# Performance work log

Measured on AMD Instinct MI355X. Metric: run time of the kernel, lower is better.

Reference implementation:

```python
import jax, jax.numpy as jnp
import numpy as np

B, T, D_MODEL, D_STATE = 8, 2048, 1024, 256


def setup_inputs() -> dict:
    key = jax.random.key(0)
    ks = jax.random.split(key, 11)
    def lecun(k, shape):
        fan_in = shape[0]
        return jax.random.normal(k, shape, jnp.float32) / jnp.sqrt(jnp.float32(fan_in))
    return {
        "x": jax.random.normal(ks[0], (B, T, D_MODEL), jnp.float32),
        "W_in": lecun(ks[1], (D_MODEL, D_STATE)),
        "b_in": jnp.zeros((D_STATE,), jnp.float32),
        "W_gate": lecun(ks[2], (D_MODEL, D_MODEL)),
        "b_gate": jnp.zeros((D_MODEL,), jnp.float32),
        "A": lecun(ks[3], (D_STATE, D_STATE)),
        "Bm": lecun(ks[4], (D_STATE, D_STATE)),
        "C": lecun(ks[5], (D_MODEL, D_STATE)),
        "D": lecun(ks[6], (D_MODEL, D_STATE)),
        "W_out": lecun(ks[7], (D_MODEL, D_MODEL)),
        "b_out": jnp.zeros((D_MODEL,), jnp.float32),
    }


def reference(x, W_in, b_in, W_gate, b_gate, A, Bm, C, D, W_out, b_out):
    b, t, d_model = x.shape
    d_state = A.shape[0]
    u = x @ W_in + b_in                      # [B,T,d_state]
    g = jax.nn.sigmoid(x @ W_gate + b_gate)  # [B,T,d_model]

    u_seq = jnp.swapaxes(u, 0, 1)  # [T,B,d_state]
    g_seq = jnp.swapaxes(g, 0, 1)  # [T,B,d_model]
    x_seq = jnp.swapaxes(x, 0, 1)  # [T,B,d_model]

    def step(h_prev, inputs):
        u_t, g_t, x_t = inputs
        h_t = jnp.tanh(h_prev @ A + u_t @ Bm)            # [B,d_state]
        y_t = h_t @ C.T + u_t @ D.T                      # [B,d_model]
        y_t = g_t * y_t + (1.0 - g_t) * x_t
        return h_t, y_t

    h0 = jnp.zeros((b, d_state), x.dtype)
    _, ys = jax.lax.scan(step, h0, xs=(u_seq, g_seq, x_seq))
    ys = jnp.swapaxes(ys, 0, 1)  # [B,T,d_model]
    return ys @ W_out + b_out + x
```

## Files before the change

kernel.cpp:

```cpp
#include <hip/hip_runtime.h>
#include <math.h>


enum { E_NONE = 0, E_BIASBF = 1, E_SIGBF = 2, E_ACC = 3, E_BIASRES = 4, E_CVTBF = 5 };

typedef __attribute__((ext_vector_type(8))) short bf16x8;
typedef __attribute__((ext_vector_type(4))) float f32x4;

static __device__ inline unsigned short f2bf(float f) {
    unsigned u = __builtin_bit_cast(unsigned, f);
    unsigned r = (u + 0x7fff + ((u >> 16) & 1)) >> 16;
    return (unsigned short)r;
}
static __device__ inline unsigned pack2(float a, float b) {
    return (unsigned)f2bf(a) | ((unsigned)f2bf(b) << 16);
}
static __device__ inline float bflo(unsigned u) {
    return __builtin_bit_cast(float, u << 16);
}
static __device__ inline float bfhi(unsigned u) {
    return __builtin_bit_cast(float, u & 0xffff0000u);
}
static __device__ inline float tanh_fast(float x) {
    float e = __builtin_amdgcn_exp2f(x * 2.8853900817779268f);
    float t = __builtin_amdgcn_rcpf(e + 1.0f);
    return fmaf(-2.0f, t, 1.0f);
}

__global__ __launch_bounds__(256) void cvt_bf(
    const float* __restrict__ in, unsigned short* __restrict__ out, int n8)
{
    int i = blockIdx.x * 256 + threadIdx.x;
    if (i >= n8) return;
    float4 a = ((const float4*)in)[i * 2];
    float4 b = ((const float4*)in)[i * 2 + 1];
    uint4 o;
    o.x = pack2(a.x, a.y); o.y = pack2(a.z, a.w);
    o.z = pack2(b.x, b.y); o.w = pack2(b.z, b.w);
    ((uint4*)out)[i] = o;
}

__global__ __launch_bounds__(256) void transpose_bf(
    const float* __restrict__ in, unsigned short* __restrict__ out, int R, int C)
{
    __shared__ float tile[32][33];
    const int bx = blockIdx.x * 32, by = blockIdx.y * 32;
    const int tx = threadIdx.x & 31, ty = threadIdx.x >> 5;
#pragma unroll
    for (int i = 0; i < 32; i += 8)
        tile[ty + i][tx] = in[(size_t)(by + ty + i) * C + bx + tx];
    __syncthreads();
#pragma unroll
    for (int i = 0; i < 32; i += 8)
        out[(size_t)(bx + ty + i) * R + by + tx] = f2bf(tile[tx][ty + i]);
}

template <int EPI>
__global__ __launch_bounds__(256) void gemm_mfma(
    const unsigned short* __restrict__ Ag,
    const unsigned short* __restrict__ Bg,
    const float* __restrict__ bias, const float* __restrict__ res,
    void* Cg, int M, int N, int K)
{
    __shared__ __align__(16) unsigned char Lds[2][32768];
    const int tid = threadIdx.x;
    const int w = tid >> 6, l = tid & 63;
    const int r = l & 15, g = l >> 4;
    const int m0 = blockIdx.y * 128, n0 = blockIdx.x * 128;

    const unsigned char* agp[4];
    const unsigned char* bgp[4];
#pragma unroll
    for (int j = 0; j < 4; ++j) {
        const int c = w * 256 + j * 64 + l;
        const int row = c >> 3;
        const unsigned offp = ((unsigned)(c & 7) * 16u) ^ ((unsigned)(row & 7) * 16u);
        agp[j] = (const unsigned char*)Ag + ((size_t)(m0 + row) * K) * 2 + offp;
        bgp[j] = (const unsigned char*)Bg + ((size_t)(n0 + row) * K) * 2 + offp;
    }

#define STAGE(BUF)                                                            \
    {                                                                         \
      _Pragma("unroll")                                                       \
      for (int j = 0; j < 4; ++j) {                                           \
        __builtin_amdgcn_global_load_lds(                                     \
            (const __attribute__((address_space(1))) unsigned*)(agp[j]),      \
            (__attribute__((address_space(3))) unsigned*)&Lds[(BUF)][w * 4096 + j * 1024], \
            16, 0, 0);                                                        \
        __builtin_amdgcn_global_load_lds(                                     \
            (const __attribute__((address_space(1))) unsigned*)(bgp[j]),      \
            (__attribute__((address_space(3))) unsigned*)&Lds[(BUF)][16384 + w * 4096 + j * 1024], \
            16, 0, 0);                                                        \
        agp[j] += 128; bgp[j] += 128;                                         \
      }                                                                       \
    }

    f32x4 acc[2][8];
#pragma unroll
    for (int mt = 0; mt < 2; ++mt)
#pragma unroll
        for (int nt = 0; nt < 8; ++nt) acc[mt][nt] = (f32x4){0.f, 0.f, 0.f, 0.f};

    const int nk = K >> 6;
    STAGE(0)
    __syncthreads();
    for (int t = 0; t < nk; ++t) {
        const int buf = t & 1;
        if (t + 1 < nk) { STAGE(buf ^ 1) }
        bf16x8 af[2][2], bfr[8][2];
#pragma unroll
        for (int s = 0; s < 2; ++s) {
#pragma unroll
            for (int mt = 0; mt < 2; ++mt) {
                const int row = w * 32 + mt * 16 + r;
                af[mt][s] = *(const bf16x8*)&Lds[buf][row * 128 +
                    ((s * 64 + 16 * g) ^ (16 * (row & 7)))];
            }
#pragma unroll
            for (int nt = 0; nt < 8; ++nt) {
                const int row = nt * 16 + r;
                bfr[nt][s] = *(const bf16x8*)&Lds[buf][16384 + row * 128 +
                    ((s * 64 + 16 * g) ^ (16 * (row & 7)))];
            }
        }
#pragma unroll
        for (int s = 0; s < 2; ++s)
#pragma unroll
            for (int mt = 0; mt < 2; ++mt)
#pragma unroll
                for (int nt = 0; nt < 8; ++nt)
                    acc[mt][nt] = __builtin_amdgcn_mfma_f32_16x16x32_bf16(
                        af[mt][s], bfr[nt][s], acc[mt][nt], 0, 0, 0);
        __syncthreads();
    }
#undef STAGE

#pragma unroll
    for (int mt = 0; mt < 2; ++mt)
#pragma unroll
        for (int nt = 0; nt < 8; ++nt) {
            const int n = n0 + nt * 16 + r;
            float bv = 0.f;
            if (EPI == E_BIASBF || EPI == E_SIGBF || EPI == E_BIASRES) bv = bias[n];
#pragma unroll
            for (int q = 0; q < 4; ++q) {
                const int m = m0 + w * 32 + mt * 16 + g * 4 + q;
                const size_t idx = (size_t)m * N + n;
                float v = acc[mt][nt][q] + bv;
                if (EPI == E_SIGBF) v = 1.f / (1.f + expf(-v));
                if (EPI == E_ACC) v += ((const float*)Cg)[idx];
                if (EPI == E_BIASRES) v += res[idx];
                if (EPI == E_BIASBF || EPI == E_SIGBF || EPI == E_CVTBF)
                    ((unsigned short*)Cg)[idx] = f2bf(v);
                else
                    ((float*)Cg)[idx] = v;
            }
        }
}

__global__ __launch_bounds__(256, 1) void scan_mfma(
    const float* __restrict__ Amat, const unsigned short* __restrict__ u2bf,
    unsigned short* __restrict__ hbf)
{
    constexpr int T = 2048;
    constexpr int NCH = T / 8;
    __shared__ __align__(16) unsigned char LDSM[8192 + 2 * 4096];
    unsigned char* Hb = LDSM;
    unsigned char* Ub = LDSM + 8192;

    const int tid = threadIdx.x;
    const int bb = blockIdx.x;
    const int w = tid >> 6, l = tid & 63;
    const int r = l & 15, g = l >> 4;
    const int m0 = w * 64;
    const bool c1 = (r & 1) != 0, c2 = (r & 2) != 0;

    if (tid < 128) ((unsigned*)Hb)[tid] = 0u;

    bf16x8 af[4][8];
#pragma unroll
    for (int mt = 0; mt < 4; ++mt) {
        const int m = m0 + mt * 16 + r;
#pragma unroll
        for (int kt = 0; kt < 8; ++kt) {
            unsigned wd[4];
#pragma unroll
            for (int jw = 0; jw < 4; ++jw) {
                const int k = kt * 32 + g * 8 + jw * 2;
                wd[jw] = pack2(Amat[(size_t)k * 256 + m],
                               Amat[(size_t)(k + 1) * 256 + m]);
            }
            af[mt][kt] = __builtin_bit_cast(bf16x8, *(uint4*)wd);
        }
    }

    const unsigned char* u2b = (const unsigned char*)u2bf + (size_t)bb * T * 512;
    unsigned short* hb = hbf + (size_t)bb * T * 256;

    __builtin_amdgcn_global_load_lds(
        (const __attribute__((address_space(1))) unsigned*)(u2b + tid * 16),
        (__attribute__((address_space(3))) unsigned*)(Ub + tid * 16), 16, 0, 0);
    __builtin_amdgcn_global_load_lds(
        (const __attribute__((address_space(1))) unsigned*)(u2b + 4096 + tid * 16),
        (__attribute__((address_space(3))) unsigned*)(Ub + 4096 + tid * 16), 16, 0, 0);
    asm volatile("s_waitcnt vmcnt(0) lgkmcnt(0)" ::: "memory");
    __builtin_amdgcn_sched_barrier(0);
    __builtin_amdgcn_s_barrier();
    __builtin_amdgcn_sched_barrier(0);

#define SCAN_STEP(I)                                                          \
  {                                                                           \
    bf16x8 hf[8];                                                             \
    _Pragma("unroll")                                                         \
    for (int kt = 0; kt < 8; ++kt)                                            \
      hf[kt] = *(const bf16x8*)(Hb + c15 + (I) * 512u +                       \
                                (unsigned)(kt * 64 + g * 16));                \
    float uu[4];                                                              \
    _Pragma("unroll")                                                         \
    for (int mt = 0; mt < 4; ++mt) {                                          \
      unsigned short us = *(const unsigned short*)(                           \
          Uc + (I) * 512u + (unsigned)((m0 + mt * 16 + g * 4 + (r & 3)) * 2));\
      uu[mt] = bflo(us);                                                      \
    }                                                                         \
    asm volatile("s_waitcnt lgkmcnt(0)" ::: "memory");                        \
    __builtin_amdgcn_sched_barrier(0);                                        \
    f32x4 p0[4], p1[4];                                                       \
    _Pragma("unroll")                                                         \
    for (int mt = 0; mt < 4; ++mt) {                                          \
      p0[mt] = (f32x4){0.f, 0.f, 0.f, 0.f};                                   \
      p1[mt] = (f32x4){0.f, 0.f, 0.f, 0.f};                                   \
    }                                                                         \
    _Pragma("unroll")                                                         \
    for (int kt = 0; kt < 4; ++kt) {                                          \
      _Pragma("unroll")                                                       \
      for (int mt = 0; mt < 4; ++mt) {                                        \
        p0[mt] = __builtin_amdgcn_mfma_f32_16x16x32_bf16(af[mt][kt], hf[kt],  \
                                                         p0[mt], 0, 0, 0);    \
        p1[mt] = __builtin_amdgcn_mfma_f32_16x16x32_bf16(                     \
            af[mt][kt + 4], hf[kt + 4], p1[mt], 0, 0, 0);                     \
      }                                                                       \
    }                                                                         \
    const unsigned bwb = ((I) == 7) ? (c15 ^ 4096u) : (c15 + ((I) + 1) * 512u);\
    _Pragma("unroll")                                                         \
    for (int mt = 0; mt < 4; ++mt) {                                          \
      float s0 = p0[mt][0] + p1[mt][0];                                       \
      float s1 = p0[mt][1] + p1[mt][1];                                       \
      float s2 = p0[mt][2] + p1[mt][2];                                       \
      float s3 = p0[mt][3] + p1[mt][3];                                       \
      float sv = c2 ? (c1 ? s3 : s2) : (c1 ? s1 : s0);                        \
      float hv = tanh_fast(sv + uu[mt]);                                      \
      unsigned pk;                                                            \
      asm("v_cvt_pk_bf16_f32 %0, %1, %2" : "=v"(pk) : "v"(hv), "v"(hv));      \
      if (r < 4)                                                              \
        *(unsigned short*)(Hb + bwb +                                         \
            (unsigned)((m0 + mt * 16 + g * 4 + r) * 2)) = (unsigned short)pk; \
    }                                                                         \
    asm volatile("s_waitcnt lgkmcnt(0)" ::: "memory");                        \
    __builtin_amdgcn_sched_barrier(0);                                        \
    __builtin_amdgcn_s_barrier();                                             \
    __builtin_amdgcn_sched_barrier(0);                                        \
  }

    for (int chunk = 0; chunk < NCH; ++chunk) {
        const int t0 = chunk * 8;
        const unsigned c15 = (unsigned)(t0 & 15) * 512u;
        unsigned char* Uc = Ub + ((unsigned)(chunk & 1) << 12);

        SCAN_STEP(0)
        SCAN_STEP(1)
        SCAN_STEP(2)
        SCAN_STEP(3)
        SCAN_STEP(4)
        SCAN_STEP(5)
        SCAN_STEP(6)
        SCAN_STEP(7)

        {
            const int flat = tid * 16;
            const int i = flat >> 9, byte = flat & 511;
            const int slot = (t0 + 1 + i) & 15;
            uint4 dat = *(const uint4*)(Hb + slot * 512 + byte);
            *(uint4*)((unsigned char*)hb + (size_t)(t0 + i) * 512 + byte) = dat;
        }
        if (chunk + 2 < NCH) {
            __builtin_amdgcn_global_load_lds(
                (const __attribute__((address_space(1))) unsigned*)(
                    u2b + (size_t)(t0 + 16) * 512 + tid * 16),
                (__attribute__((address_space(3))) unsigned*)(
                    Ub + ((unsigned)(chunk & 1) << 12) + tid * 16), 16, 0, 0);
            asm volatile("s_waitcnt vmcnt(2)" ::: "memory");
        } else {
            asm volatile("s_waitcnt vmcnt(1)" ::: "memory");
        }
        __builtin_amdgcn_sched_barrier(0);
        __builtin_amdgcn_s_barrier();
        __builtin_amdgcn_sched_barrier(0);
    }
#undef SCAN_STEP
}

__global__ __launch_bounds__(256) void ewise(
    const unsigned short* __restrict__ g8, const float* __restrict__ big,
    const float* __restrict__ x, unsigned short* __restrict__ ys, int n8)
{
    int i = blockIdx.x * 256 + threadIdx.x;
    if (i >= n8) return;
    uint4 gv = ((const uint4*)g8)[i];
    float4 b0 = ((const float4*)big)[i * 2], b1 = ((const float4*)big)[i * 2 + 1];
    float4 x0 = ((const float4*)x)[i * 2], x1 = ((const float4*)x)[i * 2 + 1];
    float gg[8] = {bflo(gv.x), bfhi(gv.x), bflo(gv.y), bfhi(gv.y),
                   bflo(gv.z), bfhi(gv.z), bflo(gv.w), bfhi(gv.w)};
    float bb[8] = {b0.x, b0.y, b0.z, b0.w, b1.x, b1.y, b1.z, b1.w};
    float xx[8] = {x0.x, x0.y, x0.z, x0.w, x1.x, x1.y, x1.z, x1.w};
    float yy[8];
#pragma unroll
    for (int k = 0; k < 8; ++k) yy[k] = gg[k] * bb[k] + (1.f - gg[k]) * xx[k];
    uint4 o;
    o.x = pack2(yy[0], yy[1]); o.y = pack2(yy[2], yy[3]);
    o.z = pack2(yy[4], yy[5]); o.w = pack2(yy[6], yy[7]);
    ((uint4*)ys)[i] = o;
}

extern "C" void kernel_launch(void* const* d_in, const int* in_sizes, int n_in,
                              void* d_out, int out_size, void* d_ws, size_t ws_size,
                              hipStream_t stream)
{
    const float* x      = (const float*)d_in[0];
    const float* W_in   = (const float*)d_in[1];
    const float* b_in   = (const float*)d_in[2];
    const float* W_gate = (const float*)d_in[3];
    const float* b_gate = (const float*)d_in[4];
    const float* Amat   = (const float*)d_in[5];
    const float* Bm     = (const float*)d_in[6];
    const float* Cm     = (const float*)d_in[7];
    const float* Dm     = (const float*)d_in[8];
    const float* W_out  = (const float*)d_in[9];
    const float* b_out  = (const float*)d_in[10];

    const int T = 2048, DM = 1024, DS = 256;
    const int M = 8 * T;
    const size_t MB = 1024 * 1024;
    char* ws = (char*)d_ws;

    unsigned short* xbf  = (unsigned short*)(ws);
    unsigned short* ysbf = xbf;
    unsigned short* u    = (unsigned short*)(ws + 32 * MB);
    unsigned short* u2   = (unsigned short*)(ws + 40 * MB);
    unsigned short* h    = (unsigned short*)(ws + 56 * MB);
    unsigned short* WinT = (unsigned short*)(ws + 64 * MB);
    unsigned short* BmT  = (unsigned short*)(ws + 64 * MB + 512 * 1024);
    unsigned short* WgT  = (unsigned short*)(ws + 65 * MB);
    unsigned short* WoT  = (unsigned short*)(ws + 67 * MB);
    unsigned short* Cbf  = (unsigned short*)(ws + 69 * MB);
    unsigned short* Dbf  = (unsigned short*)(ws + 69 * MB + 512 * 1024);
    float*          big  = (float*)(ws + 70 * MB);
    unsigned short* gbf  = (unsigned short*)(ws + 134 * MB);

    cvt_bf<<<M * DM / 8 / 256, 256, 0, stream>>>(x, xbf, M * DM / 8);
    transpose_bf<<<dim3(DS / 32, DM / 32), 256, 0, stream>>>(W_in, WinT, DM, DS);
    transpose_bf<<<dim3(DS / 32, DS / 32), 256, 0, stream>>>(Bm, BmT, DS, DS);
    transpose_bf<<<dim3(DM / 32, DM / 32), 256, 0, stream>>>(W_gate, WgT, DM, DM);
    transpose_bf<<<dim3(DM / 32, DM / 32), 256, 0, stream>>>(W_out, WoT, DM, DM);
    cvt_bf<<<DM * DS / 8 / 256, 256, 0, stream>>>(Cm, Cbf, DM * DS / 8);
    cvt_bf<<<DM * DS / 8 / 256, 256, 0, stream>>>(Dm, Dbf, DM * DS / 8);

    gemm_mfma<E_BIASBF><<<dim3(DS / 128, M / 128), 256, 0, stream>>>(
        xbf, WinT, b_in, nullptr, u, M, DS, DM);
    gemm_mfma<E_NONE><<<dim3(DM / 128, M / 128), 256, 0, stream>>>(
        u, Dbf, nullptr, nullptr, big, M, DM, DS);
    gemm_mfma<E_CVTBF><<<dim3(DS / 128, M / 128), 256, 0, stream>>>(
        u, BmT, nullptr, nullptr, u2, M, DS, DS);
    gemm_mfma<E_SIGBF><<<dim3(DM / 128, M / 128), 256, 0, stream>>>(
        xbf, WgT, b_gate, nullptr, gbf, M, DM, DM);
    scan_mfma<<<8, 256, 0, stream>>>(Amat, u2, h);
    gemm_mfma<E_ACC><<<dim3(DM / 128, M / 128), 256, 0, stream>>>(
        h, Cbf, nullptr, nullptr, big, M, DM, DS);
    ewise<<<M * DM / 8 / 256, 256, 0, stream>>>(gbf, big, x, ysbf, M * DM / 8);
    gemm_mfma<E_BIASRES><<<dim3(DM / 128, M / 128), 256, 0, stream>>>(
        ysbf, WoT, b_out, x, (float*)d_out, M, DM, DM);
}
```

Before: 1.559 ms.

## Interleave two batch recurrences per scan workgroup to hide MFMA latency

The scan kernel now processes two independent batch sequences per workgroup, launching 4 blocks instead of 8. Each step issues the MFMA chains for both sequences back to back, so one chain's latency can overlap the other, and the two sequences share a single barrier per step. The cost is double the per-step work on each block, more LDS and registers, and half as many compute units in use.

```diff
diff --git a/kernel.cpp b/kernel.cpp
--- a/kernel.cpp
+++ b/kernel.cpp
@@ -164,18 +164,23 @@
 {
     constexpr int T = 2048;
     constexpr int NCH = T / 8;
-    __shared__ __align__(16) unsigned char LDSM[8192 + 2 * 4096];
-    unsigned char* Hb = LDSM;
-    unsigned char* Ub = LDSM + 8192;
+    __shared__ __align__(16) unsigned char LDSM[4 * 8192];
+    unsigned char* HbA = LDSM;
+    unsigned char* HbB = LDSM + 8192;
+    unsigned char* UA  = LDSM + 16384;
+    unsigned char* UB  = LDSM + 24576;
 
     const int tid = threadIdx.x;
-    const int bb = blockIdx.x;
+    const int p = blockIdx.x;
     const int w = tid >> 6, l = tid & 63;
     const int r = l & 15, g = l >> 4;
     const int m0 = w * 64;
     const bool c1 = (r & 1) != 0, c2 = (r & 2) != 0;
 
-    if (tid < 128) ((unsigned*)Hb)[tid] = 0u;
+    if (tid < 128) {
+        ((unsigned*)HbA)[tid] = 0u;
+        ((unsigned*)HbB)[tid] = 0u;
+    }
 
     bf16x8 af[4][8];
 #pragma unroll
@@ -194,66 +199,97 @@
         }
     }
 
-    const unsigned char* u2b = (const unsigned char*)u2bf + (size_t)bb * T * 512;
-    unsigned short* hb = hbf + (size_t)bb * T * 256;
-
-    __builtin_amdgcn_global_load_lds(
-        (const __attribute__((address_space(1))) unsigned*)(u2b + tid * 16),
-        (__attribute__((address_space(3))) unsigned*)(Ub + tid * 16), 16, 0, 0);
-    __builtin_amdgcn_global_load_lds(
-        (const __attribute__((address_space(1))) unsigned*)(u2b + 4096 + tid * 16),
-        (__attribute__((address_space(3))) unsigned*)(Ub + 4096 + tid * 16), 16, 0, 0);
-    asm volatile("s_waitcnt vmcnt(0) lgkmcnt(0)" ::: "memory");
+    const unsigned char* uAsrc = (const unsigned char*)u2bf + (size_t)(2 * p) * T * 512;
+    const unsigned char* uBsrc = (const unsigned char*)u2bf + (size_t)(2 * p + 1) * T * 512;
+    unsigned char* hAdst = (unsigned char*)(hbf + (size_t)(2 * p) * T * 256);
+    unsigned char* hBdst = (unsigned char*)(hbf + (size_t)(2 * p + 1) * T * 256);
+
+#pragma unroll
+    for (int buf = 0; buf < 2; ++buf) {
+        __builtin_amdgcn_global_load_lds(
+            (const __attribute__((address_space(1))) unsigned*)(uAsrc + buf * 4096 + tid * 16),
+            (__attribute__((address_space(3))) unsigned*)(UA + buf * 4096 + tid * 16), 16, 0, 0);
+        __builtin_amdgcn_global_load_lds(
+            (const __attribute__((address_space(1))) unsigned*)(uBsrc + buf * 4096 + tid * 16),
+            (__attribute__((address_space(3))) unsigned*)(UB + buf * 4096 + tid * 16), 16, 0, 0);
+    }
+    asm volatile("s_waitcnt vmcnt(2) lgkmcnt(0)" ::: "memory");
     __builtin_amdgcn_sched_barrier(0);
     __builtin_amdgcn_s_barrier();
     __builtin_amdgcn_sched_barrier(0);
 
+    unsigned uo[4];
+#pragma unroll
+    for (int mt = 0; mt < 4; ++mt)
+        uo[mt] = (unsigned)((m0 + mt * 16 + g * 4 + (r & 3)) * 2);
+
+#define CHAIN(HB, UC, PF0, PF1, US)                                           \
+    {                                                                         \
+      _Pragma("unroll")                                                       \
+      for (int mt = 0; mt < 4; ++mt) {                                        \
+        PF0[mt] = (f32x4){0.f, 0.f, 0.f, 0.f};                                \
+        PF1[mt] = (f32x4){0.f, 0.f, 0.f, 0.f};                                \
+      }                                                                       \
+    }
+
 #define SCAN_STEP(I)                                                          \
   {                                                                           \
-    bf16x8 hf[8];                                                             \
+    const unsigned ro = c15 + (I) * 512u;                                     \
+    const unsigned bwb = ((I) == 7) ? (c15 ^ 4096u) : (c15 + ((I) + 1) * 512u);\
+    bf16x8 hfA[8], hfB[8];                                                    \
     _Pragma("unroll")                                                         \
     for (int kt = 0; kt < 8; ++kt)                                            \
-      hf[kt] = *(const bf16x8*)(Hb + c15 + (I) * 512u +                       \
-                                (unsigned)(kt * 64 + g * 16));                \
-    float uu[4];                                                              \
+      hfA[kt] = *(const bf16x8*)(HbA + ro + (unsigned)(kt * 64 + g * 16));    \
+    _Pragma("unroll")                                                         \
+    for (int kt = 0; kt < 8; ++kt)                                            \
+      hfB[kt] = *(const bf16x8*)(HbB + ro + (unsigned)(kt * 64 + g * 16));    \
+    unsigned short usA[4], usB[4];                                            \
     _Pragma("unroll")                                                         \
     for (int mt = 0; mt < 4; ++mt) {                                          \
-      unsigned short us = *(const unsigned short*)(                           \
-          Uc + (I) * 512u + (unsigned)((m0 + mt * 16 + g * 4 + (r & 3)) * 2));\
-      uu[mt] = bflo(us);                                                      \
+      usA[mt] = *(const unsigned short*)(UcA + (I) * 512u + uo[mt]);          \
+      usB[mt] = *(const unsigned short*)(UcB + (I) * 512u + uo[mt]);          \
     }                                                                         \
-    asm volatile("s_waitcnt lgkmcnt(0)" ::: "memory");                        \
-    __builtin_amdgcn_sched_barrier(0);                                        \
-    f32x4 p0[4], p1[4];                                                       \
-    _Pragma("unroll")                                                         \
-    for (int mt = 0; mt < 4; ++mt) {                                          \
-      p0[mt] = (f32x4){0.f, 0.f, 0.f, 0.f};                                   \
-      p1[mt] = (f32x4){0.f, 0.f, 0.f, 0.f};                                   \
-    }                                                                         \
+    f32x4 pA0[4], pA1[4], pB0[4], pB1[4];                                     \
+    CHAIN(HbA, UcA, pA0, pA1, usA)                                            \
+    CHAIN(HbB, UcB, pB0, pB1, usB)                                            \
     _Pragma("unroll")                                                         \
     for (int kt = 0; kt < 4; ++kt) {                                          \
       _Pragma("unroll")                                                       \
       for (int mt = 0; mt < 4; ++mt) {                                        \
-        p0[mt] = __builtin_amdgcn_mfma_f32_16x16x32_bf16(af[mt][kt], hf[kt],  \
-                                                         p0[mt], 0, 0, 0);    \
-        p1[mt] = __builtin_amdgcn_mfma_f32_16x16x32_bf16(                     \
-            af[mt][kt + 4], hf[kt + 4], p1[mt], 0, 0, 0);                     \
+        pA0[mt] = __builtin_amdgcn_mfma_f32_16x16x32_bf16(af[mt][kt], hfA[kt],\
+                                                          pA0[mt], 0, 0, 0);  \
+        pA1[mt] = __builtin_amdgcn_mfma_f32_16x16x32_bf16(                    \
+            af[mt][kt + 4], hfA[kt + 4], pA1[mt], 0, 0, 0);                   \
       }                                                                       \
     }                                                                         \
-    const unsigned bwb = ((I) == 7) ? (c15 ^ 4096u) : (c15 + ((I) + 1) * 512u);\
+    _Pragma("unroll")                                                         \
+    for (int kt = 0; kt < 4; ++kt) {                                          \
+      _Pragma("unroll")                                                       \
+      for (int mt = 0; mt < 4; ++mt) {                                        \
+        pB0[mt] = __builtin_amdgcn_mfma_f32_16x16x32_bf16(af[mt][kt], hfB[kt],\
+                                                          pB0[mt], 0, 0, 0);  \
+        pB1[mt] = __builtin_amdgcn_mfma_f32_16x16x32_bf16(                    \
+            af[mt][kt + 4], hfB[kt + 4], pB1[mt], 0, 0, 0);                   \
+      }                                                                       \
+    }                                                                         \
     _Pragma("unroll")                                                         \
     for (int mt = 0; mt < 4; ++mt) {                                          \
-      float s0 = p0[mt][0] + p1[mt][0];                                       \
-      float s1 = p0[mt][1] + p1[mt][1];                                       \
-      float s2 = p0[mt][2] + p1[mt][2];                                       \
-      float s3 = p0[mt][3] + p1[mt][3];                                       \
-      float sv = c2 ? (c1 ? s3 : s2) : (c1 ? s1 : s0);                        \
-      float hv = tanh_fast(sv + uu[mt]);                                      \
-      unsigned pk;                                                            \
-      asm("v_cvt_pk_bf16_f32 %0, %1, %2" : "=v"(pk) : "v"(hv), "v"(hv));      \
-      if (r < 4)                                                              \
-        *(unsigned short*)(Hb + bwb +                                         \
-            (unsigned)((m0 + mt * 16 + g * 4 + r) * 2)) = (unsigned short)pk; \
+      float a0 = pA0[mt][0] + pA1[mt][0], a1 = pA0[mt][1] + pA1[mt][1];       \
+      float a2 = pA0[mt][2] + pA1[mt][2], a3 = pA0[mt][3] + pA1[mt][3];       \
+      float sa = c2 ? (c1 ? a3 : a2) : (c1 ? a1 : a0);                        \
+      float ha = tanh_fast(sa + bflo((unsigned)usA[mt]));                     \
+      float b0 = pB0[mt][0] + pB1[mt][0], b1 = pB0[mt][1] + pB1[mt][1];       \
+      float b2 = pB0[mt][2] + pB1[mt][2], b3 = pB0[mt][3] + pB1[mt][3];       \
+      float sb = c2 ? (c1 ? b3 : b2) : (c1 ? b1 : b0);                        \
+      float hbv = tanh_fast(sb + bflo((unsigned)usB[mt]));                    \
+      unsigned pka, pkb;                                                      \
+      asm("v_cvt_pk_bf16_f32 %0, %1, %2" : "=v"(pka) : "v"(ha), "v"(ha));     \
+      asm("v_cvt_pk_bf16_f32 %0, %1, %2" : "=v"(pkb) : "v"(hbv), "v"(hbv));   \
+      if (r < 4) {                                                            \
+        const unsigned wb = bwb + (unsigned)((m0 + mt * 16 + g * 4 + r) * 2); \
+        *(unsigned short*)(HbA + wb) = (unsigned short)pka;                   \
+        *(unsigned short*)(HbB + wb) = (unsigned short)pkb;                   \
+      }                                                                       \
     }                                                                         \
     asm volatile("s_waitcnt lgkmcnt(0)" ::: "memory");                        \
     __builtin_amdgcn_sched_barrier(0);                                        \
@@ -264,7 +300,8 @@
     for (int chunk = 0; chunk < NCH; ++chunk) {
         const int t0 = chunk * 8;
         const unsigned c15 = (unsigned)(t0 & 15) * 512u;
-        unsigned char* Uc = Ub + ((unsigned)(chunk & 1) << 12);
+        const unsigned char* UcA = UA + ((unsigned)(chunk & 1) << 12);
+        const unsigned char* UcB = UB + ((unsigned)(chunk & 1) << 12);
 
         SCAN_STEP(0)
         SCAN_STEP(1)
@@ -276,27 +313,34 @@
         SCAN_STEP(7)
 
         {
-            const int flat = tid * 16;
-            const int i = flat >> 9, byte = flat & 511;
+            const int i = tid >> 5;
+            const int byte = (tid & 31) * 16;
             const int slot = (t0 + 1 + i) & 15;
-            uint4 dat = *(const uint4*)(Hb + slot * 512 + byte);
-            *(uint4*)((unsigned char*)hb + (size_t)(t0 + i) * 512 + byte) = dat;
+            uint4 da = *(const uint4*)(HbA + slot * 512 + byte);
+            uint4 db = *(const uint4*)(HbB + slot * 512 + byte);
+            *(uint4*)(hAdst + (size_t)(t0 + i) * 512 + byte) = da;
+            *(uint4*)(hBdst + (size_t)(t0 + i) * 512 + byte) = db;
         }
         if (chunk + 2 < NCH) {
+            const unsigned nb = (unsigned)(chunk & 1) << 12;
             __builtin_amdgcn_global_load_lds(
                 (const __attribute__((address_space(1))) unsigned*)(
-                    u2b + (size_t)(t0 + 16) * 512 + tid * 16),
-                (__attribute__((address_space(3))) unsigned*)(
-                    Ub + ((unsigned)(chunk & 1) << 12) + tid * 16), 16, 0, 0);
+                    uAsrc + (size_t)(t0 + 16) * 512 + tid * 16),
+                (__attribute__((address_space(3))) unsigned*)(UA + nb + tid * 16), 16, 0, 0);
+            __builtin_amdgcn_global_load_lds(
+                (const __attribute__((address_space(1))) unsigned*)(
+                    uBsrc + (size_t)(t0 + 16) * 512 + tid * 16),
+                (__attribute__((address_space(3))) unsigned*)(UB + nb + tid * 16), 16, 0, 0);
+            asm volatile("s_waitcnt vmcnt(4)" ::: "memory");
+        } else {
             asm volatile("s_waitcnt vmcnt(2)" ::: "memory");
-        } else {
-            asm volatile("s_waitcnt vmcnt(1)" ::: "memory");
         }
         __builtin_amdgcn_sched_barrier(0);
         __builtin_amdgcn_s_barrier();
         __builtin_amdgcn_sched_barrier(0);
     }
 #undef SCAN_STEP
+#undef CHAIN
 }
 
 __global__ __launch_bounds__(256) void ewise(
@@ -372,7 +416,7 @@
         u, BmT, nullptr, nullptr, u2, M, DS, DS);
     gemm_mfma<E_SIGBF><<<dim3(DM / 128, M / 128), 256, 0, stream>>>(
         xbf, WgT, b_gate, nullptr, gbf, M, DM, DM);
-    scan_mfma<<<8, 256, 0, stream>>>(Amat, u2, h);
+    scan_mfma<<<4, 256, 0, stream>>>(Amat, u2, h);
     gemm_mfma<E_ACC><<<dim3(DM / 128, M / 128), 256, 0, stream>>>(
         h, Cbf, nullptr, nullptr, big, M, DM, DS);
     ewise<<<M * DM / 8 / 256, 256, 0, stream>>>(gbf, big, x, ysbf, M * DM / 8);
```

Result: slower. 2.746 ms (+76.1%).

## Batch all sequences into one scan workgroup using MFMA N dimension

Applied to the files above, without the earlier changes.

The recurrent scan goes from eight single-batch workgroups to one 512-thread workgroup. The eight batch rows now fill the MFMA column dimension, with batches duplicated across the 16 columns. Each wave owns 32 state rows instead of 64, which halves the serial MFMA chain per timestep. The h and u buffers move to a swizzled, per-step layout that packs two outputs per lane and drops the per-lane select. In exchange, the whole scan runs on a single CU with a larger LDS footprint and an 8-wave barrier every chunk.

```diff
diff --git a/kernel.cpp b/kernel.cpp
--- a/kernel.cpp
+++ b/kernel.cpp
@@ -158,28 +158,28 @@
         }
 }
 
-__global__ __launch_bounds__(256, 1) void scan_mfma(
+__global__ __launch_bounds__(512, 2) void scan_mfma(
     const float* __restrict__ Amat, const unsigned short* __restrict__ u2bf,
     unsigned short* __restrict__ hbf)
 {
     constexpr int T = 2048;
     constexpr int NCH = T / 8;
-    __shared__ __align__(16) unsigned char LDSM[8192 + 2 * 4096];
+    __shared__ __align__(16) unsigned char LDSM[131072];
     unsigned char* Hb = LDSM;
-    unsigned char* Ub = LDSM + 8192;
+    unsigned char* Ub = LDSM + 65536;
 
     const int tid = threadIdx.x;
-    const int bb = blockIdx.x;
     const int w = tid >> 6, l = tid & 63;
-    const int r = l & 15, g = l >> 4;
-    const int m0 = w * 64;
-    const bool c1 = (r & 1) != 0, c2 = (r & 2) != 0;
-
-    if (tid < 128) ((unsigned*)Hb)[tid] = 0u;
-
-    bf16x8 af[4][8];
-#pragma unroll
-    for (int mt = 0; mt < 4; ++mt) {
+    const int r = l & 15, g = l >> 4, r8 = r & 7;
+    const bool hi = (r & 8) != 0;
+    const int m0 = w * 32;
+
+    ((unsigned*)Hb)[tid] = 0u;
+    ((unsigned*)Hb)[tid + 512] = 0u;
+
+    bf16x8 af[2][8];
+#pragma unroll
+    for (int mt = 0; mt < 2; ++mt) {
         const int m = m0 + mt * 16 + r;
 #pragma unroll
         for (int kt = 0; kt < 8; ++kt) {
@@ -194,15 +194,38 @@
         }
     }
 
-    const unsigned char* u2b = (const unsigned char*)u2bf + (size_t)bb * T * 512;
-    unsigned short* hb = hbf + (size_t)bb * T * 256;
-
-    __builtin_amdgcn_global_load_lds(
-        (const __attribute__((address_space(1))) unsigned*)(u2b + tid * 16),
-        (__attribute__((address_space(3))) unsigned*)(Ub + tid * 16), 16, 0, 0);
-    __builtin_amdgcn_global_load_lds(
-        (const __attribute__((address_space(1))) unsigned*)(u2b + 4096 + tid * 16),
-        (__attribute__((address_space(3))) unsigned*)(Ub + 4096 + tid * 16), 16, 0, 0);
+    unsigned ubase[2], woff[2];
+#pragma unroll
+    for (int mt = 0; mt < 2; ++mt) {
+        const int s0 = m0 + mt * 16 + g * 4;
+        const int s = s0 + (hi ? 2 : 0);
+        ubase[mt] = (unsigned)(r8 * 512 + (((s >> 3) ^ r8) * 16) + (s & 7) * 2);
+        woff[mt] = (unsigned)((((s0 >> 5) * 32 + ((s0 >> 3) & 3) * 8 + r8) * 16)
+                              + ((s0 & 7) + (hi ? 2 : 0)) * 2);
+    }
+    const unsigned rbase = (unsigned)((g * 8 + r8) * 16);
+
+    int sg_i[4], sg_b[4], sg_kg[4];
+#pragma unroll
+    for (int j = 0; j < 4; ++j) {
+        const int d = j * 512 + tid;
+        sg_i[j] = d >> 8;
+        sg_b[j] = (d >> 5) & 7;
+        sg_kg[j] = (d & 31) ^ sg_b[j];
+    }
+
+#pragma unroll
+    for (int c0 = 0; c0 < 2; ++c0)
+#pragma unroll
+        for (int j = 0; j < 4; ++j) {
+            const size_t srcb = ((size_t)(sg_b[j] * T + c0 * 8 + sg_i[j]) * 512)
+                              + (unsigned)(sg_kg[j] * 16);
+            __builtin_amdgcn_global_load_lds(
+                (const __attribute__((address_space(1))) unsigned*)(
+                    (const unsigned char*)u2bf + srcb),
+                (__attribute__((address_space(3))) unsigned*)(
+                    Ub + c0 * 32768 + (j * 512 + tid) * 16), 16, 0, 0);
+        }
     asm volatile("s_waitcnt vmcnt(0) lgkmcnt(0)" ::: "memory");
     __builtin_amdgcn_sched_barrier(0);
     __builtin_amdgcn_s_barrier();
@@ -210,50 +233,41 @@
 
 #define SCAN_STEP(I)                                                          \
   {                                                                           \
+    const unsigned sr = ((unsigned)(t0 + (I)) & 15u) * 4096u;                 \
+    const unsigned sw = ((unsigned)(t0 + (I) + 1) & 15u) * 4096u;             \
     bf16x8 hf[8];                                                             \
     _Pragma("unroll")                                                         \
     for (int kt = 0; kt < 8; ++kt)                                            \
-      hf[kt] = *(const bf16x8*)(Hb + c15 + (I) * 512u +                       \
-                                (unsigned)(kt * 64 + g * 16));                \
-    float uu[4];                                                              \
+      hf[kt] = *(const bf16x8*)(Hb + sr + rbase + (unsigned)(kt * 512));      \
+    unsigned uv[2];                                                           \
     _Pragma("unroll")                                                         \
-    for (int mt = 0; mt < 4; ++mt) {                                          \
-      unsigned short us = *(const unsigned short*)(                           \
-          Uc + (I) * 512u + (unsigned)((m0 + mt * 16 + g * 4 + (r & 3)) * 2));\
-      uu[mt] = bflo(us);                                                      \
-    }                                                                         \
-    asm volatile("s_waitcnt lgkmcnt(0)" ::: "memory");                        \
-    __builtin_amdgcn_sched_barrier(0);                                        \
-    f32x4 p0[4], p1[4];                                                       \
+    for (int mt = 0; mt < 2; ++mt)                                            \
+      uv[mt] = *(const unsigned*)(Uc + (unsigned)(I) * 4096u + ubase[mt]);    \
+    f32x4 p0[2], p1[2];                                                       \
     _Pragma("unroll")                                                         \
-    for (int mt = 0; mt < 4; ++mt) {                                          \
+    for (int mt = 0; mt < 2; ++mt) {                                          \
       p0[mt] = (f32x4){0.f, 0.f, 0.f, 0.f};                                   \
       p1[mt] = (f32x4){0.f, 0.f, 0.f, 0.f};                                   \
     }                                                                         \
     _Pragma("unroll")                                                         \
     for (int kt = 0; kt < 4; ++kt) {                                          \
       _Pragma("unroll")                                                       \
-      for (int mt = 0; mt < 4; ++mt) {                                        \
+      for (int mt = 0; mt < 2; ++mt) {                                        \
         p0[mt] = __builtin_amdgcn_mfma_f32_16x16x32_bf16(af[mt][kt], hf[kt],  \
                                                          p0[mt], 0, 0, 0);    \
         p1[mt] = __builtin_amdgcn_mfma_f32_16x16x32_bf16(                     \
             af[mt][kt + 4], hf[kt + 4], p1[mt], 0, 0, 0);                     \
       }                                                                       \
     }                                                                         \
-    const unsigned bwb = ((I) == 7) ? (c15 ^ 4096u) : (c15 + ((I) + 1) * 512u);\
     _Pragma("unroll")                                                         \
-    for (int mt = 0; mt < 4; ++mt) {                                          \
-      float s0 = p0[mt][0] + p1[mt][0];                                       \
-      float s1 = p0[mt][1] + p1[mt][1];                                       \
-      float s2 = p0[mt][2] + p1[mt][2];                                       \
-      float s3 = p0[mt][3] + p1[mt][3];                                       \
-      float sv = c2 ? (c1 ? s3 : s2) : (c1 ? s1 : s0);                        \
-      float hv = tanh_fast(sv + uu[mt]);                                      \
+    for (int mt = 0; mt < 2; ++mt) {                                          \
+      const float slo = hi ? (p0[mt][2] + p1[mt][2]) : (p0[mt][0] + p1[mt][0]);\
+      const float shi = hi ? (p0[mt][3] + p1[mt][3]) : (p0[mt][1] + p1[mt][1]);\
+      const float h0 = tanh_fast(slo + bflo(uv[mt]));                         \
+      const float h1 = tanh_fast(shi + bfhi(uv[mt]));                         \
       unsigned pk;                                                            \
-      asm("v_cvt_pk_bf16_f32 %0, %1, %2" : "=v"(pk) : "v"(hv), "v"(hv));      \
-      if (r < 4)                                                              \
-        *(unsigned short*)(Hb + bwb +                                         \
-            (unsigned)((m0 + mt * 16 + g * 4 + r) * 2)) = (unsigned short)pk; \
+      asm("v_cvt_pk_bf16_f32 %0, %1, %2" : "=v"(pk) : "v"(h0), "v"(h1));      \
+      *(unsigned*)(Hb + sw + woff[mt]) = pk;                                  \
     }                                                                         \
     asm volatile("s_waitcnt lgkmcnt(0)" ::: "memory");                        \
     __builtin_amdgcn_sched_barrier(0);                                        \
@@ -263,8 +277,7 @@
 
     for (int chunk = 0; chunk < NCH; ++chunk) {
         const int t0 = chunk * 8;
-        const unsigned c15 = (unsigned)(t0 & 15) * 512u;
-        unsigned char* Uc = Ub + ((unsigned)(chunk & 1) << 12);
+        const unsigned char* Uc = Ub + ((unsigned)(chunk & 1) << 15);
 
         SCAN_STEP(0)
         SCAN_STEP(1)
@@ -276,25 +289,38 @@
         SCAN_STEP(7)
 
         {
-            const int flat = tid * 16;
-            const int i = flat >> 9, byte = flat & 511;
-            const int slot = (t0 + 1 + i) & 15;
-            uint4 dat = *(const uint4*)(Hb + slot * 512 + byte);
-            *(uint4*)((unsigned char*)hb + (size_t)(t0 + i) * 512 + byte) = dat;
+#pragma unroll
+            for (int j = 0; j < 4; ++j) {
+                const int p = j * 512 + tid;
+                const int di = p >> 8, wp = p & 255;
+                const int kt_ = wp >> 5, sl_ = wp & 31;
+                const unsigned slot = (unsigned)((t0 + 1 + di) & 15) * 4096u;
+                uint4 dat = *(const uint4*)(Hb + slot + (unsigned)wp * 16u);
+                const size_t off = ((size_t)((sl_ & 7) * T + t0 + di) * 256 +
+                                    kt_ * 32 + (sl_ >> 3) * 8);
+                *(uint4*)(hbf + off) = dat;
+            }
+            if (chunk + 2 < NCH) {
+                const unsigned nb = (unsigned)(chunk & 1) << 15;
+#pragma unroll
+                for (int j = 0; j < 4; ++j) {
+                    const size_t srcb =
+                        ((size_t)(sg_b[j] * T + t0 + 16 + sg_i[j]) * 512)
+                        + (unsigned)(sg_kg[j] * 16);
+                    __builtin_amdgcn_global_load_lds(
+                        (const __attribute__((address_space(1))) unsigned*)(
+                            (const unsigned char*)u2bf + srcb),
+                        (__attribute__((address_space(3))) unsigned*)(
+                            Ub + nb + (j * 512 + tid) * 16), 16, 0, 0);
+                }
+                asm volatile("s_waitcnt vmcnt(8) lgkmcnt(0)" ::: "memory");
+            } else {
+                asm volatile("s_waitcnt vmcnt(4) lgkmcnt(0)" ::: "memory");
+            }
+            __builtin_amdgcn_sched_barrier(0);
+            __builtin_amdgcn_s_barrier();
+            __builtin_amdgcn_sched_barrier(0);
         }
-        if (chunk + 2 < NCH) {
-            __builtin_amdgcn_global_load_lds(
-                (const __attribute__((address_space(1))) unsigned*)(
-                    u2b + (size_t)(t0 + 16) * 512 + tid * 16),
-                (__attribute__((address_space(3))) unsigned*)(
-                    Ub + ((unsigned)(chunk & 1) << 12) + tid * 16), 16, 0, 0);
-            asm volatile("s_waitcnt vmcnt(2)" ::: "memory");
-        } else {
-            asm volatile("s_waitcnt vmcnt(1)" ::: "memory");
-        }
-        __builtin_amdgcn_sched_barrier(0);
-        __builtin_amdgcn_s_barrier();
-        __builtin_amdgcn_sched_barrier(0);
     }
 #undef SCAN_STEP
 }
@@ -372,7 +398,7 @@
         u, BmT, nullptr, nullptr, u2, M, DS, DS);
     gemm_mfma<E_SIGBF><<<dim3(DM / 128, M / 128), 256, 0, stream>>>(
         xbf, WgT, b_gate, nullptr, gbf, M, DM, DM);
-    scan_mfma<<<8, 256, 0, stream>>>(Amat, u2, h);
+    scan_mfma<<<1, 512, 0, stream>>>(Amat, u2, h);
     gemm_mfma<E_ACC><<<dim3(DM / 128, M / 128), 256, 0, stream>>>(
         h, Cbf, nullptr, nullptr, big, M, DM, DS);
     ewise<<<M * DM / 8 / 256, 256, 0, stream>>>(gbf, big, x, ysbf, M * DM / 8);
```

Measured after the change: 1.540 ms. No clear change (-1.3%).
